# Optimization experiments

Measured on AMD Instinct MI355X. Metric: run time of the kernel, lower is better.

The kernel has to match this reference:

```python
import jax, jax.numpy as jnp
import numpy as np

TEMP = 0.1
TEMP_SUP = 0.5
PROP = 0.5  # proportion_pure_contrastive
SIGMA = 1.0
GAMMA = 1.0 / (2.0 * SIGMA ** 2)
INF = 1e8


def _l2norm(x, eps=1e-12):
    # torch F.normalize: x / max(||x||, eps)
    n = jnp.sqrt(jnp.sum(x * x, axis=-1, keepdims=True))
    return x / jnp.maximum(n, eps)


def _cross_entropy(logits, targets):
    # mean over rows of -log_softmax(logits)[i, targets[i]]
    logp = jax.nn.log_softmax(logits, axis=-1)
    return -jnp.mean(jnp.take_along_axis(logp, targets[:, None], axis=-1))


def setup_inputs() -> dict:
    key = jax.random.key(0)
    k1, k2, k3 = jax.random.split(key, 3)
    N, D = 4096, 256
    z_i = jax.random.normal(k1, (N, D), dtype=jnp.float32)
    z_j = jax.random.normal(k2, (N, D), dtype=jnp.float32)
    labels = jax.random.normal(k3, (N, 1), dtype=jnp.float32)
    return {"z_i": z_i, "z_j": z_j, "labels": labels}


def _forward(z_i, z_j, labels):
    N = z_i.shape[0]
    eye = jnp.eye(N, dtype=z_i.dtype)
    zin = _l2norm(z_i)
    zjn = _l2norm(z_j)

    # ---- pure contrastive branch (temperature TEMP) ----
    sim_zii = zin @ zin.T / TEMP - INF * eye
    sim_zjj = zjn @ zjn.T / TEMP - INF * eye
    sim_zij = zin @ zjn.T / TEMP
    correct = jnp.arange(N, dtype=jnp.int32)
    loss_i = _cross_entropy(jnp.concatenate([sim_zij, sim_zii], axis=1), correct)
    loss_j = _cross_entropy(jnp.concatenate([sim_zij.T, sim_zjj], axis=1), correct)
    loss_pure = loss_i + loss_j

    # ---- supervised branch (temperature TEMP_SUP) ----
    s_zii = zin @ zin.T / TEMP_SUP - INF * eye
    s_zjj = zjn @ zjn.T / TEMP_SUP - INF * eye
    s_zij = zin @ zjn.T / TEMP_SUP

    # RBF kernel on duplicated labels (detached in original -> stop_gradient)
    all_lab = jnp.tile(labels.reshape(N, -1), (2, 1))  # [2N, L]
    all_lab = jax.lax.stop_gradient(all_lab)
    sq = jnp.sum(all_lab * all_lab, axis=1)
    d2 = sq[:, None] + sq[None, :] - 2.0 * (all_lab @ all_lab.T)
    weights = jnp.exp(-GAMMA * jnp.maximum(d2, 0.0))  # [2N, 2N]
    weights = weights * (1.0 - jnp.eye(2 * N, dtype=weights.dtype))
    norm = jnp.sum(weights, axis=1, keepdims=True)  # [2N, 1]
    weights = weights / norm
    weights_norm = weights * jnp.log(norm)

    sim_Z = jnp.concatenate([
        jnp.concatenate([s_zii, s_zij], axis=1),
        jnp.concatenate([s_zij.T, s_zjj], axis=1),
    ], axis=0)  # [2N, 2N]
    log_sim_Z = jax.nn.log_softmax(sim_Z, axis=1)
    loss_sup = (-1.0 / N) * jnp.sum(weights * log_sim_Z)
    loss_sup += (-1.0 / N) * jnp.sum(weights_norm)

    return PROP * loss_pure + (1.0 - PROP) * loss_sup


def reference(z_i, z_j, labels):
    return _forward(z_i, z_j, labels)
```

## Files before the change

kernel.cpp:

```cpp
#include <hip/hip_runtime.h>
#include <hip/hip_bf16.h>

#define NN 4096
#define DD 256
#define CCN 8
#define TPB 16
#define LOG2E 1.44269504088896f

typedef __attribute__((ext_vector_type(8))) short bf16x8;
typedef __attribute__((ext_vector_type(4))) float f32x4;
typedef __attribute__((ext_vector_type(2))) float f32x2;

typedef const unsigned int __attribute__((address_space(1)))* gu32p;
typedef unsigned int __attribute__((address_space(3)))* su32p;

__device__ __forceinline__ float fexp2(float x) { return __builtin_amdgcn_exp2f(x); }

__global__ __launch_bounds__(256) void k_norm(const float* __restrict__ zi,
                                              const float* __restrict__ zj,
                                              const float* __restrict__ labels,
                                              __hip_bfloat16* __restrict__ oi,
                                              __hip_bfloat16* __restrict__ oj,
                                              float* __restrict__ T,
                                              float* __restrict__ out) {
  __shared__ float Tred[2][2];
  if (blockIdx.x == 0 && threadIdx.x == 0) out[0] = 0.f;
  int gw = (blockIdx.x * 256 + threadIdx.x) >> 6;
  int lane = threadIdx.x & 63;
  int wave = threadIdx.x >> 6;
  const float* src = (gw < NN) ? zi : zj;
  __hip_bfloat16* dst = (gw < NN) ? oi : oj;
  int row = (gw < NN) ? gw : gw - NN;
  float4 v = ((const float4*)(src + (size_t)row * DD))[lane];
  float ss = v.x * v.x + v.y * v.y + v.z * v.z + v.w * v.w;
#pragma unroll
  for (int m = 1; m < 64; m <<= 1) ss += __shfl_xor(ss, m);
  float s = 1.0f / fmaxf(sqrtf(ss), 1e-12f);
  __hip_bfloat16* d = dst + (size_t)row * DD + lane * 4;
  d[0] = __float2bfloat16(v.x * s);
  d[1] = __float2bfloat16(v.y * s);
  d[2] = __float2bfloat16(v.z * s);
  d[3] = __float2bfloat16(v.w * s);

  {
    int r = blockIdx.x * 2 + (wave & 1);
    int h = wave >> 1;
    float lr = labels[r];
    float acc = 0.f;
    for (int it = h * 32; it < h * 32 + 32; ++it) {
      float dl = lr - labels[it * 64 + lane];
      acc += fexp2(dl * dl * (-0.5f * LOG2E));
    }
#pragma unroll
    for (int m = 1; m < 64; m <<= 1) acc += __shfl_xor(acc, m);
    if (lane == 0) Tred[wave & 1][h] = acc;
  }
  __syncthreads();
  if (threadIdx.x < 2)
    T[blockIdx.x * 2 + threadIdx.x] = Tred[threadIdx.x][0] + Tred[threadIdx.x][1];
}

template <int MODE, bool COL>
__device__ __forceinline__ void epi(
    const f32x4 acc[2][2], const f32x2 labr[2][2], const float* __restrict__ labels,
    f32x2 rA[2][2], f32x2 rB[2][2], f32x2 rC[2][2],
    f32x2 cw2[2][3], float* __restrict__ diag,
    int rowbase, int colbase, int wave, int fr, int kg) {
#pragma unroll
  for (int cf = 0; cf < 2; ++cf) {
    const int cg = colbase + cf * 16 + fr;
    const float labc = labels[cg];
    const f32x2 labc2 = {labc, labc};
#pragma unroll
    for (int sub = 0; sub < 2; ++sub) {
#pragma unroll
      for (int pp = 0; pp < 2; ++pp) {
        f32x2 S = {acc[sub][cf][2 * pp], acc[sub][cf][2 * pp + 1]};
        f32x2 arg = S * (2.f * LOG2E) + (-2.f * LOG2E);
        f32x2 b;
        b.x = fexp2(arg.x);
        b.y = fexp2(arg.y);
        f32x2 b2 = b * b;
        f32x2 b5 = b2 * b2 * b;
        f32x2 dl = labr[sub][pp] - labc2;
        f32x2 e = (dl * (-0.5f * LOG2E)) * dl;
        f32x2 kk;
        kk.x = fexp2(e.x);
        kk.y = fexp2(e.y);
        f32x2 ks = kk * S;
        if (MODE != 0) {
          const int rg = rowbase + wave * 32 + sub * 16 + kg * 4 + 2 * pp;
          if (MODE == 1) {
            if (rg == cg) diag[cg] = S.x;
            if (rg + 1 == cg) diag[cg] = S.y;
          } else {
            if (rg == cg)     { b5.x = 0.f; b.x = 0.f; ks.x = 0.f; }
            if (rg + 1 == cg) { b5.y = 0.f; b.y = 0.f; ks.y = 0.f; }
          }
        }
        rA[sub][pp] += b5;
        rB[sub][pp] += b;
        rC[sub][pp] += ks;
        if (COL) {
          cw2[cf][0] += b5;
          cw2[cf][1] += b;
          cw2[cf][2] += ks;
        }
      }
    }
  }
}

__global__ __launch_bounds__(256, 2) void k_main(
    const __hip_bfloat16* __restrict__ zin, const __hip_bfloat16* __restrict__ zjn,
    const float* __restrict__ labels,
    float* __restrict__ part, float* __restrict__ colp, float* __restrict__ diag) {
  __shared__ short lB[2][32 * 256];

  const int cc = blockIdx.x;
  const int by = blockIdx.y;
  const int combo = blockIdx.z;
  const bool COLF = (combo == 0);

  const __hip_bfloat16* Ap = (combo == 2) ? zjn : zin;
  const __hip_bfloat16* Bp = (combo == 1) ? zin : zjn;

  const int tid = threadIdx.x;
  const int lane = tid & 63;
  const int wave = tid >> 6;
  const int fr = lane & 15;
  const int kg = lane >> 4;
  const int rowbase = by * 128;
  char* lBc = (char*)lB;

  bf16x8 a[2][8];
#pragma unroll
  for (int sub = 0; sub < 2; ++sub) {
    const __hip_bfloat16* Ar =
        Ap + (size_t)(rowbase + wave * 32 + sub * 16 + fr) * DD + kg * 8;
#pragma unroll
    for (int k = 0; k < 8; ++k) a[sub][k] = *(const bf16x8*)(Ar + k * 32);
  }

  f32x2 labr[2][2];
#pragma unroll
  for (int sub = 0; sub < 2; ++sub)
#pragma unroll
    for (int pp = 0; pp < 2; ++pp) {
      const float* lp = labels + rowbase + wave * 32 + sub * 16 + kg * 4 + 2 * pp;
      labr[sub][pp] = (f32x2){lp[0], lp[1]};
    }

  f32x2 rA[2][2] = {}, rB[2][2] = {}, rC[2][2] = {};

  const int frb = (fr >> 2) & 1;
  const int P0 = fr * 512 + ((kg ^ (fr & 3)) << 4) + (frb << 6);

#define STAGE(t, buf)                                                         \
  {                                                                           \
    const char* Bt = (const char*)Bp + (size_t)(cc * 512 + (t) * 32) * 512;   \
    char* dst = lBc + (buf) * 16384;                                          \
    _Pragma("unroll") for (int j = 0; j < 4; ++j) {                           \
      int f = tid + 256 * j;                                                  \
      int g = f ^ ((f >> 5) & 7);                                             \
      __builtin_amdgcn_global_load_lds(                                       \
          (gu32p)(const void*)(Bt + (size_t)g * 16),                          \
          (su32p)(void*)(dst + (wave * 64 + 256 * j) * 16), 16, 0, 0);        \
    }                                                                         \
  }

  auto do_mfma = [&](f32x4 (&ACC)[2][2], const char* cur) {
#pragma unroll
    for (int s2 = 0; s2 < 2; ++s2)
#pragma unroll
      for (int cf = 0; cf < 2; ++cf) ACC[s2][cf] = (f32x4){0.f, 0.f, 0.f, 0.f};
#pragma unroll
    for (int k = 0; k < 8; ++k) {
      const char* bbase = cur + (P0 ^ (k << 6));
#pragma unroll
      for (int cf = 0; cf < 2; ++cf) {
        bf16x8 bv = *(const bf16x8*)(bbase + cf * 8192);
        ACC[0][cf] = __builtin_amdgcn_mfma_f32_16x16x32_bf16(a[0][k], bv, ACC[0][cf], 0, 0, 0);
        ACC[1][cf] = __builtin_amdgcn_mfma_f32_16x16x32_bf16(a[1][k], bv, ACC[1][cf], 0, 0, 0);
      }
    }
  };

  auto do_epi = [&](const f32x4 (&ACC)[2][2], int te) {
    const int colbase = cc * 512 + te * 32;
    const unsigned dtt = (unsigned)(te + 16 * cc - 4 * by);
    f32x2 cw2[2][3] = {};
    if (COLF) {
      if (dtt < 4u)
        epi<1, true>(ACC, labr, labels, rA, rB, rC, cw2, diag, rowbase, colbase, wave, fr, kg);
      else
        epi<0, true>(ACC, labr, labels, rA, rB, rC, cw2, diag, rowbase, colbase, wave, fr, kg);
      float* cp = colp + ((size_t)(by * 128 + cc * TPB + te) * 4 + wave) * 96;
#pragma unroll
      for (int cf = 0; cf < 2; ++cf)
#pragma unroll
        for (int p = 0; p < 3; ++p) {
          float v = cw2[cf][p].x + cw2[cf][p].y;
          v += __shfl_xor(v, 16);
          v += __shfl_xor(v, 32);
          if (kg == 0) cp[p * 32 + cf * 16 + fr] = v;
        }
    } else {
      if (dtt < 4u)
        epi<2, false>(ACC, labr, labels, rA, rB, rC, cw2, diag, rowbase, colbase, wave, fr, kg);
      else
        epi<0, false>(ACC, labr, labels, rA, rB, rC, cw2, diag, rowbase, colbase, wave, fr, kg);
    }
  };

  f32x4 accA[2][2], accB[2][2];

  STAGE(0, 0);
  __syncthreads();

#pragma unroll
  for (int tt = 0; tt < TPB / 2; ++tt) {
    const int t0 = 2 * tt, t1 = 2 * tt + 1;
    STAGE(t0 + 1, 1);
    if (t0 > 0) do_epi(accB, t0 - 1);
    do_mfma(accA, lBc);
    __syncthreads();

    if (t1 < TPB - 1) STAGE(t1 + 1, 0);
    do_epi(accA, t0);
    do_mfma(accB, lBc + 16384);
    __syncthreads();
  }
  do_epi(accB, TPB - 1);

  float* pc = part + (size_t)cc * 9 * NN;
  const int pr = combo;
#pragma unroll
  for (int sub = 0; sub < 2; ++sub)
#pragma unroll
    for (int pp = 0; pp < 2; ++pp)
#pragma unroll
      for (int comp = 0; comp < 2; ++comp) {
        float va = rA[sub][pp][comp], vb = rB[sub][pp][comp], vc = rC[sub][pp][comp];
#pragma unroll
        for (int m = 1; m < 16; m <<= 1) {
          va += __shfl_xor(va, m);
          vb += __shfl_xor(vb, m);
          vc += __shfl_xor(vc, m);
        }
        if (fr == 0) {
          int r = rowbase + wave * 32 + sub * 16 + kg * 4 + 2 * pp + comp;
          pc[pr * NN + r] = va;
          pc[(3 + pr) * NN + r] = vb;
          pc[(6 + pr) * NN + r] = vc;
        }
      }
}

__global__ __launch_bounds__(256) void k_final(
    const float* __restrict__ part, const float* __restrict__ colp,
    const float* __restrict__ diag, const float* __restrict__ T,
    float* __restrict__ out) {
  int r = blockIdx.x * 64 + (threadIdx.x >> 2);
  int q = threadIdx.x & 3;
  float st[9];
#pragma unroll
  for (int p = 0; p < 9; ++p) {
    float s = 0.f;
#pragma unroll
    for (int c = 0; c < CCN; ++c) s += part[((size_t)c * 9 + p) * NN + r];
    st[p] = s;
  }
  float a3 = 0.f, b3 = 0.f, c3 = 0.f;
  const int cct = r >> 5, c31 = r & 31;
  for (int by = 8 * q; by < 8 * q + 8; ++by) {
    const float* cp = colp + (size_t)(by * 128 + cct) * 4 * 96;
#pragma unroll
    for (int w = 0; w < 4; ++w) {
      a3 += cp[w * 96 + c31];
      b3 += cp[w * 96 + 32 + c31];
      c3 += cp[w * 96 + 64 + c31];
    }
  }
  a3 += __shfl_xor(a3, 1); a3 += __shfl_xor(a3, 2);
  b3 += __shfl_xor(b3, 1); b3 += __shfl_xor(b3, 2);
  c3 += __shfl_xor(c3, 1); c3 += __shfl_xor(c3, 2);

  float v = 0.f;
  if (q == 0) {
    float d = diag[r];
    float accP = logf(st[0] + st[1]) + logf(a3 + st[2]) + 20.f - 20.f * d;
    float nrm = 2.f * T[r] - 1.f;
    float W = 2.f * (st[6] + st[7] + c3 + st[8]) / nrm;
    float accS = logf(st[3] + st[4]) + logf(b3 + st[5]) + 4.f - W - 2.f * logf(nrm);
    v = accP + accS;
  }
#pragma unroll
  for (int m = 1; m < 64; m <<= 1) v += __shfl_xor(v, m);
  __shared__ float red[4];
  if ((threadIdx.x & 63) == 0) red[threadIdx.x >> 6] = v;
  __syncthreads();
  if (threadIdx.x == 0)
    atomicAdd(out, 0.5f * (red[0] + red[1] + red[2] + red[3]) / (float)NN);
}

extern "C" void kernel_launch(void* const* d_in, const int* in_sizes, int n_in,
                              void* d_out, int out_size, void* d_ws, size_t ws_size,
                              hipStream_t stream) {
  const float* zi = (const float*)d_in[0];
  const float* zj = (const float*)d_in[1];
  const float* labels = (const float*)d_in[2];
  float* out = (float*)d_out;

  char* ws = (char*)d_ws;
  __hip_bfloat16* zinH = (__hip_bfloat16*)ws;
  __hip_bfloat16* zjnH = (__hip_bfloat16*)(ws + (size_t)NN * DD * 2);
  float* part = (float*)(ws + (size_t)NN * DD * 4);
  float* colp = part + (size_t)CCN * 9 * NN;
  float* diag = colp + (size_t)4096 * 4 * 96;
  float* T = diag + NN;

  k_norm<<<2 * NN / 4, 256, 0, stream>>>(zi, zj, labels, zinH, zjnH, T, out);

  dim3 grid(CCN, NN / 128, 3);
  k_main<<<grid, 256, 0, stream>>>(zinH, zjnH, labels, part, colp, diag);

  k_final<<<NN / 64, 256, 0, stream>>>(part, colp, diag, T, out);
}
```

Baseline: 70.50 us.

## Split main kernel rows across eight waves with sixteen rows each

New measurement: 82.91 us. +17.6%, slower.

```diff
diff --git a/kernel.cpp b/kernel.cpp
--- a/kernel.cpp
+++ b/kernel.cpp
@@ -62,8 +62,8 @@
 
 template <int MODE, bool COL>
 __device__ __forceinline__ void epi(
-    const f32x4 acc[2][2], const f32x2 labr[2][2], const float* __restrict__ labels,
-    f32x2 rA[2][2], f32x2 rB[2][2], f32x2 rC[2][2],
+    const f32x4 acc[2], const f32x2 labr[2], const float* __restrict__ labels,
+    f32x2 rA[2], f32x2 rB[2], f32x2 rC[2],
     f32x2 cw2[2][3], float* __restrict__ diag,
     int rowbase, int colbase, int wave, int fr, int kg) {
 #pragma unroll
@@ -72,46 +72,43 @@
     const float labc = labels[cg];
     const f32x2 labc2 = {labc, labc};
 #pragma unroll
-    for (int sub = 0; sub < 2; ++sub) {
-#pragma unroll
-      for (int pp = 0; pp < 2; ++pp) {
-        f32x2 S = {acc[sub][cf][2 * pp], acc[sub][cf][2 * pp + 1]};
-        f32x2 arg = S * (2.f * LOG2E) + (-2.f * LOG2E);
-        f32x2 b;
-        b.x = fexp2(arg.x);
-        b.y = fexp2(arg.y);
-        f32x2 b2 = b * b;
-        f32x2 b5 = b2 * b2 * b;
-        f32x2 dl = labr[sub][pp] - labc2;
-        f32x2 e = (dl * (-0.5f * LOG2E)) * dl;
-        f32x2 kk;
-        kk.x = fexp2(e.x);
-        kk.y = fexp2(e.y);
-        f32x2 ks = kk * S;
-        if (MODE != 0) {
-          const int rg = rowbase + wave * 32 + sub * 16 + kg * 4 + 2 * pp;
-          if (MODE == 1) {
-            if (rg == cg) diag[cg] = S.x;
-            if (rg + 1 == cg) diag[cg] = S.y;
-          } else {
-            if (rg == cg)     { b5.x = 0.f; b.x = 0.f; ks.x = 0.f; }
-            if (rg + 1 == cg) { b5.y = 0.f; b.y = 0.f; ks.y = 0.f; }
-          }
+    for (int pp = 0; pp < 2; ++pp) {
+      f32x2 S = {acc[cf][2 * pp], acc[cf][2 * pp + 1]};
+      f32x2 arg = S * (2.f * LOG2E) + (-2.f * LOG2E);
+      f32x2 b;
+      b.x = fexp2(arg.x);
+      b.y = fexp2(arg.y);
+      f32x2 b2 = b * b;
+      f32x2 b5 = b2 * b2 * b;
+      f32x2 dl = labr[pp] - labc2;
+      f32x2 e = (dl * (-0.5f * LOG2E)) * dl;
+      f32x2 kk;
+      kk.x = fexp2(e.x);
+      kk.y = fexp2(e.y);
+      f32x2 ks = kk * S;
+      if (MODE != 0) {
+        const int rg = rowbase + wave * 16 + kg * 4 + 2 * pp;
+        if (MODE == 1) {
+          if (rg == cg) diag[cg] = S.x;
+          if (rg + 1 == cg) diag[cg] = S.y;
+        } else {
+          if (rg == cg)     { b5.x = 0.f; b.x = 0.f; ks.x = 0.f; }
+          if (rg + 1 == cg) { b5.y = 0.f; b.y = 0.f; ks.y = 0.f; }
         }
-        rA[sub][pp] += b5;
-        rB[sub][pp] += b;
-        rC[sub][pp] += ks;
-        if (COL) {
-          cw2[cf][0] += b5;
-          cw2[cf][1] += b;
-          cw2[cf][2] += ks;
-        }
-      }
-    }
-  }
-}
-
-__global__ __launch_bounds__(256, 2) void k_main(
+      }
+      rA[pp] += b5;
+      rB[pp] += b;
+      rC[pp] += ks;
+      if (COL) {
+        cw2[cf][0] += b5;
+        cw2[cf][1] += b;
+        cw2[cf][2] += ks;
+      }
+    }
+  }
+}
+
+__global__ __launch_bounds__(512, 2) void k_main(
     const __hip_bfloat16* __restrict__ zin, const __hip_bfloat16* __restrict__ zjn,
     const float* __restrict__ labels,
     float* __restrict__ part, float* __restrict__ colp, float* __restrict__ diag) {
@@ -133,25 +130,22 @@
   const int rowbase = by * 128;
   char* lBc = (char*)lB;
 
-  bf16x8 a[2][8];
-#pragma unroll
-  for (int sub = 0; sub < 2; ++sub) {
+  bf16x8 a[8];
+  {
     const __hip_bfloat16* Ar =
-        Ap + (size_t)(rowbase + wave * 32 + sub * 16 + fr) * DD + kg * 8;
-#pragma unroll
-    for (int k = 0; k < 8; ++k) a[sub][k] = *(const bf16x8*)(Ar + k * 32);
-  }
-
-  f32x2 labr[2][2];
-#pragma unroll
-  for (int sub = 0; sub < 2; ++sub)
-#pragma unroll
-    for (int pp = 0; pp < 2; ++pp) {
-      const float* lp = labels + rowbase + wave * 32 + sub * 16 + kg * 4 + 2 * pp;
-      labr[sub][pp] = (f32x2){lp[0], lp[1]};
-    }
-
-  f32x2 rA[2][2] = {}, rB[2][2] = {}, rC[2][2] = {};
+        Ap + (size_t)(rowbase + wave * 16 + fr) * DD + kg * 8;
+#pragma unroll
+    for (int k = 0; k < 8; ++k) a[k] = *(const bf16x8*)(Ar + k * 32);
+  }
+
+  f32x2 labr[2];
+#pragma unroll
+  for (int pp = 0; pp < 2; ++pp) {
+    const float* lp = labels + rowbase + wave * 16 + kg * 4 + 2 * pp;
+    labr[pp] = (f32x2){lp[0], lp[1]};
+  }
+
+  f32x2 rA[2] = {}, rB[2] = {}, rC[2] = {};
 
   const int frb = (fr >> 2) & 1;
   const int P0 = fr * 512 + ((kg ^ (fr & 3)) << 4) + (frb << 6);
@@ -160,33 +154,30 @@
   {                                                                           \
     const char* Bt = (const char*)Bp + (size_t)(cc * 512 + (t) * 32) * 512;   \
     char* dst = lBc + (buf) * 16384;                                          \
-    _Pragma("unroll") for (int j = 0; j < 4; ++j) {                           \
-      int f = tid + 256 * j;                                                  \
+    _Pragma("unroll") for (int j = 0; j < 2; ++j) {                           \
+      int f = tid + 512 * j;                                                  \
       int g = f ^ ((f >> 5) & 7);                                             \
       __builtin_amdgcn_global_load_lds(                                       \
           (gu32p)(const void*)(Bt + (size_t)g * 16),                          \
-          (su32p)(void*)(dst + (wave * 64 + 256 * j) * 16), 16, 0, 0);        \
+          (su32p)(void*)(dst + (wave * 64 + 512 * j) * 16), 16, 0, 0);        \
     }                                                                         \
   }
 
-  auto do_mfma = [&](f32x4 (&ACC)[2][2], const char* cur) {
-#pragma unroll
-    for (int s2 = 0; s2 < 2; ++s2)
-#pragma unroll
-      for (int cf = 0; cf < 2; ++cf) ACC[s2][cf] = (f32x4){0.f, 0.f, 0.f, 0.f};
+  auto do_mfma = [&](f32x4 (&ACC)[2], const char* cur) {
+#pragma unroll
+    for (int cf = 0; cf < 2; ++cf) ACC[cf] = (f32x4){0.f, 0.f, 0.f, 0.f};
 #pragma unroll
     for (int k = 0; k < 8; ++k) {
       const char* bbase = cur + (P0 ^ (k << 6));
 #pragma unroll
       for (int cf = 0; cf < 2; ++cf) {
         bf16x8 bv = *(const bf16x8*)(bbase + cf * 8192);
-        ACC[0][cf] = __builtin_amdgcn_mfma_f32_16x16x32_bf16(a[0][k], bv, ACC[0][cf], 0, 0, 0);
-        ACC[1][cf] = __builtin_amdgcn_mfma_f32_16x16x32_bf16(a[1][k], bv, ACC[1][cf], 0, 0, 0);
+        ACC[cf] = __builtin_amdgcn_mfma_f32_16x16x32_bf16(a[k], bv, ACC[cf], 0, 0, 0);
       }
     }
   };
 
-  auto do_epi = [&](const f32x4 (&ACC)[2][2], int te) {
+  auto do_epi = [&](const f32x4 (&ACC)[2], int te) {
     const int colbase = cc * 512 + te * 32;
     const unsigned dtt = (unsigned)(te + 16 * cc - 4 * by);
     f32x2 cw2[2][3] = {};
@@ -195,7 +186,7 @@
         epi<1, true>(ACC, labr, labels, rA, rB, rC, cw2, diag, rowbase, colbase, wave, fr, kg);
       else
         epi<0, true>(ACC, labr, labels, rA, rB, rC, cw2, diag, rowbase, colbase, wave, fr, kg);
-      float* cp = colp + ((size_t)(by * 128 + cc * TPB + te) * 4 + wave) * 96;
+      float* cp = colp + ((size_t)(by * 128 + cc * TPB + te) * 8 + wave) * 96;
 #pragma unroll
       for (int cf = 0; cf < 2; ++cf)
 #pragma unroll
@@ -213,7 +204,7 @@
     }
   };
 
-  f32x4 accA[2][2], accB[2][2];
+  f32x4 accA[2], accB[2];
 
   STAGE(0, 0);
   __syncthreads();
@@ -236,25 +227,23 @@
   float* pc = part + (size_t)cc * 9 * NN;
   const int pr = combo;
 #pragma unroll
-  for (int sub = 0; sub < 2; ++sub)
-#pragma unroll
-    for (int pp = 0; pp < 2; ++pp)
-#pragma unroll
-      for (int comp = 0; comp < 2; ++comp) {
-        float va = rA[sub][pp][comp], vb = rB[sub][pp][comp], vc = rC[sub][pp][comp];
-#pragma unroll
-        for (int m = 1; m < 16; m <<= 1) {
-          va += __shfl_xor(va, m);
-          vb += __shfl_xor(vb, m);
-          vc += __shfl_xor(vc, m);
-        }
-        if (fr == 0) {
-          int r = rowbase + wave * 32 + sub * 16 + kg * 4 + 2 * pp + comp;
-          pc[pr * NN + r] = va;
-          pc[(3 + pr) * NN + r] = vb;
-          pc[(6 + pr) * NN + r] = vc;
-        }
-      }
+  for (int pp = 0; pp < 2; ++pp)
+#pragma unroll
+    for (int comp = 0; comp < 2; ++comp) {
+      float va = rA[pp][comp], vb = rB[pp][comp], vc = rC[pp][comp];
+#pragma unroll
+      for (int m = 1; m < 16; m <<= 1) {
+        va += __shfl_xor(va, m);
+        vb += __shfl_xor(vb, m);
+        vc += __shfl_xor(vc, m);
+      }
+      if (fr == 0) {
+        int r = rowbase + wave * 16 + kg * 4 + 2 * pp + comp;
+        pc[pr * NN + r] = va;
+        pc[(3 + pr) * NN + r] = vb;
+        pc[(6 + pr) * NN + r] = vc;
+      }
+    }
 }
 
 __global__ __launch_bounds__(256) void k_final(
@@ -274,9 +263,9 @@
   float a3 = 0.f, b3 = 0.f, c3 = 0.f;
   const int cct = r >> 5, c31 = r & 31;
   for (int by = 8 * q; by < 8 * q + 8; ++by) {
-    const float* cp = colp + (size_t)(by * 128 + cct) * 4 * 96;
-#pragma unroll
-    for (int w = 0; w < 4; ++w) {
+    const float* cp = colp + (size_t)(by * 128 + cct) * 8 * 96;
+#pragma unroll
+    for (int w = 0; w < 8; ++w) {
       a3 += cp[w * 96 + c31];
       b3 += cp[w * 96 + 32 + c31];
       c3 += cp[w * 96 + 64 + c31];
@@ -317,13 +306,13 @@
   __hip_bfloat16* zjnH = (__hip_bfloat16*)(ws + (size_t)NN * DD * 2);
   float* part = (float*)(ws + (size_t)NN * DD * 4);
   float* colp = part + (size_t)CCN * 9 * NN;
-  float* diag = colp + (size_t)4096 * 4 * 96;
+  float* diag = colp + (size_t)4096 * 8 * 96;
   float* T = diag + NN;
 
   k_norm<<<2 * NN / 4, 256, 0, stream>>>(zi, zj, labels, zinH, zjnH, T, out);
 
   dim3 grid(CCN, NN / 128, 3);
-  k_main<<<grid, 256, 0, stream>>>(zinH, zjnH, labels, part, colp, diag);
+  k_main<<<grid, 512, 0, stream>>>(zinH, zjnH, labels, part, colp, diag);
 
   k_final<<<NN / 64, 256, 0, stream>>>(part, colp, diag, T, out);
 }
```
